# Kernel optimization log

Hardware: AMD Instinct MI355X
Metric: run time of the kernel (lower is better)

Reference implementation:

```python
import jax, jax.numpy as jnp
import numpy as np

T = 16            # hardcoded timesteps in DQSN.forward
V_TH = 1.0        # IFNode default v_threshold
TAU = 2.0         # NonSpikingLIFNode tau
SG_ALPHA = 4.0    # spikingjelly surrogate.Sigmoid alpha


@jax.custom_vjp
def spike_fn(x):
    # Heaviside step with sigmoid surrogate gradient (spikingjelly default).
    return (x >= 0.0).astype(x.dtype)

def _spike_fwd(x):
    return spike_fn(x), x

def _spike_bwd(x, g):
    s = jax.nn.sigmoid(SG_ALPHA * x)
    return (g * SG_ALPHA * s * (1.0 - s),)

spike_fn.defvjp(_spike_fwd, _spike_bwd)


def setup_inputs() -> dict:
    key = jax.random.key(0)
    ks = jax.random.split(key, 5)
    B, H = 16384, 4096
    x = jax.random.normal(ks[0], (B, 4), dtype=jnp.float32)
    W1 = jax.random.normal(ks[1], (H, 4), dtype=jnp.float32) * 0.5   # Linear(4, H)
    b1 = jax.random.normal(ks[2], (H,), dtype=jnp.float32) * 0.1
    W2 = jax.random.normal(ks[3], (2, H), dtype=jnp.float32) * 0.02  # Linear(H, 2)
    b2 = jax.random.normal(ks[4], (2,), dtype=jnp.float32) * 0.1
    return {"x": x, "W1": W1, "b1": b1, "W2": W2, "b2": b2}


def reference(x, W1, b1, W2, b2):
    B = x.shape[0]
    H = W1.shape[0]
    # Input current is constant across the T steps (same x every step).
    I1 = x @ W1.T + b1                        # [B, H]

    def step(carry, _):
        v1, v2 = carry
        # IFNode: charge, spike (hard reset to v_reset=0)
        v1 = v1 + I1
        s = spike_fn(v1 - V_TH)               # [B, H]
        v1 = v1 * (1.0 - s)
        # Linear(H, 2) -> NonSpikingLIFNode: v += (dv - (v - 0)) / tau
        dv = s @ W2.T + b2                    # [B, 2]
        v2 = v2 + (dv - v2) / TAU
        return (v1, v2), None

    v1_0 = jnp.zeros((B, H), dtype=x.dtype)
    v2_0 = jnp.zeros((B, 2), dtype=x.dtype)
    (v1, v2), _ = jax.lax.scan(step, (v1_0, v2_0), None, length=T)
    return v2
```

## Files before the change

### kernel.cpp

```cpp
#include <hip/hip_runtime.h>


constexpr int TSTEPS = 16;
constexpr int NB = 8;
constexpr float GUARD = 4e-5f;
constexpr float GTHR  = 0.5f - GUARD;

__global__ __launch_bounds__(256) void dqsn_fwd(
    const float* __restrict__ x,
    const float* __restrict__ W1,
    const float* __restrict__ b1,
    const float* __restrict__ W2,
    const float* __restrict__ b2,
    float* __restrict__ out,
    int B, int H)
{
    const int tid  = threadIdx.x;
    const int lane = tid & 63;
    const int b0   = blockIdx.x * NB;

    float tval = 0.0f;
    if (lane >= 1 && lane <= TSTEPS) {
        unsigned mm = 0;
        for (int k = lane; k <= TSTEPS; k += lane) mm |= 1u << (k - 1);
        tval = (float)mm * 0x1p-16f;
    }
    const int table_reg = __float_as_int(tval);

    float xs0[NB], xs1[NB], xs2[NB], xs3[NB];
#pragma unroll
    for (int i = 0; i < NB; ++i) {
        const int bi = (b0 + i < B) ? (b0 + i) : (B - 1);
        xs0[i] = x[bi * 4 + 0];
        xs1[i] = x[bi * 4 + 1];
        xs2[i] = x[bi * 4 + 2];
        xs3[i] = x[bi * 4 + 3];
    }

    float acc0[NB], acc1[NB];
#pragma unroll
    for (int i = 0; i < NB; ++i) { acc0[i] = 0.0f; acc1[i] = 0.0f; }

    for (int h = tid; h < H; h += 256) {
        const float4 w1 = *reinterpret_cast<const float4*>(W1 + (size_t)h * 4);
        const float bb  = b1[h];
        const float w2a = W2[h];
        const float w2b = W2[H + h];

#pragma unroll
        for (int i = 0; i < NB; ++i) {
            const float I = fmaf(xs0[i], w1.x,
                            fmaf(xs1[i], w1.y,
                            fmaf(xs2[i], w1.z,
                            fmaf(xs3[i], w1.w, bb))));

            const float r = __builtin_amdgcn_rcpf(I);
            const float c = __builtin_ceilf(r);
            int idx = (int)__builtin_amdgcn_fmed3f(c, 0.0f, 17.0f) << 2;

            if (__builtin_expect(
                    (unsigned long long)__ballot(fabsf((r - c) + 0.5f) > GTHR), 0)) {
                float v = 0.0f;
                int cnt = 0;
#pragma unroll
                for (int t = 0; t < TSTEPS; ++t) {
                    v += I;
                    cnt += (v < 1.0f) ? 1 : 0;
                }
                idx = (cnt + 1) << 2;
            }

            const float A = __int_as_float(__builtin_amdgcn_ds_bpermute(idx, table_reg));
            acc0[i] = fmaf(A, w2a, acc0[i]);
            acc1[i] = fmaf(A, w2b, acc1[i]);
        }
    }

    float v[16];
#pragma unroll
    for (int i = 0; i < NB; ++i) {
        v[2 * i + 0] = acc0[i];
        v[2 * i + 1] = acc1[i];
    }

    {
        const bool up = (lane & 32) != 0;
#pragma unroll
        for (int k = 0; k < 8; ++k) {
            const float mine = up ? v[k] : v[k + 8];
            const float recv = __shfl_xor(mine, 32, 64);
            v[k] = (up ? v[k + 8] : v[k]) + recv;
        }
    }
    {
        const bool up = (lane & 16) != 0;
#pragma unroll
        for (int k = 0; k < 4; ++k) {
            const float mine = up ? v[k] : v[k + 4];
            const float recv = __shfl_xor(mine, 16, 64);
            v[k] = (up ? v[k + 4] : v[k]) + recv;
        }
    }
    {
        const bool up = (lane & 8) != 0;
#pragma unroll
        for (int k = 0; k < 2; ++k) {
            const float mine = up ? v[k] : v[k + 2];
            const float recv = __shfl_xor(mine, 8, 64);
            v[k] = (up ? v[k + 2] : v[k]) + recv;
        }
    }
    {
        const bool up = (lane & 4) != 0;
        const float mine = up ? v[0] : v[1];
        const float recv = __shfl_xor(mine, 4, 64);
        v[0] = (up ? v[1] : v[0]) + recv;
    }
    float tot = v[0];
    tot += __shfl_xor(tot, 1, 64);
    tot += __shfl_xor(tot, 2, 64);

    __shared__ float red[4][16];
    if ((lane & 3) == 0) red[tid >> 6][lane >> 2] = tot;
    __syncthreads();

    if (tid < 16) {
        const float s = (red[0][tid] + red[1][tid]) + (red[2][tid] + red[3][tid]);
        const int i = tid >> 1;
        const int o = tid & 1;
        if (b0 + i < B)
            out[(b0 + i) * 2 + o] = s + b2[o] * (1.0f - 0x1p-16f);
    }
}

extern "C" void kernel_launch(void* const* d_in, const int* in_sizes, int n_in,
                              void* d_out, int out_size, void* d_ws, size_t ws_size,
                              hipStream_t stream) {
    const float* x  = (const float*)d_in[0];
    const float* W1 = (const float*)d_in[1];
    const float* b1 = (const float*)d_in[2];
    const float* W2 = (const float*)d_in[3];
    const float* b2 = (const float*)d_in[4];
    float* out = (float*)d_out;

    const int B = in_sizes[0] / 4;
    const int H = in_sizes[2];

    const int grid = (B + NB - 1) / NB;
    dqsn_fwd<<<grid, 256, 0, stream>>>(x, W1, b1, W2, b2, out, B, H);
}
```

Baseline: 31.94 us.

## Split hidden dimension across two blocks and add a combine kernel

Each batch tile is now processed by two blocks, each covering half of the hidden dimension and writing partial sums to workspace. A second small kernel adds the two partials and the bias. The intent is more blocks for better load balance and occupancy. In exchange it adds a kernel launch, a workspace round trip, and duplicated per-block setup and reduction.

```diff
diff --git a/kernel.cpp b/kernel.cpp
--- a/kernel.cpp
+++ b/kernel.cpp
@@ -6,18 +6,21 @@
 constexpr float GUARD = 4e-5f;
 constexpr float GTHR  = 0.5f - GUARD;
 
-__global__ __launch_bounds__(256) void dqsn_fwd(
+__global__ __launch_bounds__(256) void dqsn_stage1(
     const float* __restrict__ x,
     const float* __restrict__ W1,
     const float* __restrict__ b1,
     const float* __restrict__ W2,
-    const float* __restrict__ b2,
-    float* __restrict__ out,
+    float* __restrict__ ws,
     int B, int H)
 {
     const int tid  = threadIdx.x;
     const int lane = tid & 63;
-    const int b0   = blockIdx.x * NB;
+    const int g    = blockIdx.x;
+    const int b0   = (g >> 1) * NB;
+    const int half = g & 1;
+    const int hbeg = half * (H >> 1);
+    const int hend = hbeg + (H >> 1);
 
     float tval = 0.0f;
     if (lane >= 1 && lane <= TSTEPS) {
@@ -41,7 +44,7 @@
 #pragma unroll
     for (int i = 0; i < NB; ++i) { acc0[i] = 0.0f; acc1[i] = 0.0f; }
 
-    for (int h = tid; h < H; h += 256) {
+    for (int h = hbeg + tid; h < hend; h += 256) {
         const float4 w1 = *reinterpret_cast<const float4*>(W1 + (size_t)h * 4);
         const float bb  = b1[h];
         const float w2a = W2[h];
@@ -126,11 +129,24 @@
 
     if (tid < 16) {
         const float s = (red[0][tid] + red[1][tid]) + (red[2][tid] + red[3][tid]);
-        const int i = tid >> 1;
-        const int o = tid & 1;
-        if (b0 + i < B)
-            out[(b0 + i) * 2 + o] = s + b2[o] * (1.0f - 0x1p-16f);
+        ws[(size_t)g * 16 + tid] = s;
     }
+}
+
+__global__ __launch_bounds__(256) void dqsn_combine(
+    const float* __restrict__ ws,
+    const float* __restrict__ b2,
+    float* __restrict__ out,
+    int B)
+{
+    const int i = blockIdx.x * 256 + threadIdx.x;
+    if (i >= B * 2) return;
+    const int b  = i >> 1;
+    const int o  = i & 1;
+    const int rg = b >> 3;
+    const int j  = ((b & 7) << 1) | o;
+    const float s = ws[(size_t)rg * 32 + j] + ws[(size_t)rg * 32 + 16 + j];
+    out[i] = s + b2[o] * (1.0f - 0x1p-16f);
 }
 
 extern "C" void kernel_launch(void* const* d_in, const int* in_sizes, int n_in,
@@ -142,10 +158,14 @@
     const float* W2 = (const float*)d_in[3];
     const float* b2 = (const float*)d_in[4];
     float* out = (float*)d_out;
+    float* ws  = (float*)d_ws;
 
     const int B = in_sizes[0] / 4;
     const int H = in_sizes[2];
 
-    const int grid = (B + NB - 1) / NB;
-    dqsn_fwd<<<grid, 256, 0, stream>>>(x, W1, b1, W2, b2, out, B, H);
+    const int grid1 = ((B + NB - 1) / NB) * 2;
+    dqsn_stage1<<<grid1, 256, 0, stream>>>(x, W1, b1, W2, ws, B, H);
+
+    const int grid2 = (B * 2 + 255) / 256;
+    dqsn_combine<<<grid2, 256, 0, stream>>>(ws, b2, out, B);
 }
```

Result: slower. 33.48 us (+4.8%).
